# Kernel optimization log

Hardware: AMD Instinct MI355X
Metric: run time of the kernel (lower is better)

Reference implementation:

```python
import jax, jax.numpy as jnp
import numpy as np

DIM = 1024
HDS = 16
HEAD_DIM = DIM // HDS
ISC = True


def setup_inputs() -> dict:
    key = jax.random.key(0)
    k = jax.random.split(key, 5)
    x = jax.random.normal(k[0], (4, 2048, DIM), dtype=jnp.float32)
    # Linear(dim, 3*dim): weight [3*dim, dim] (torch layout), bias [3*dim]
    scale = 1.0 / np.sqrt(DIM)
    w_qkv = jax.random.uniform(k[1], (3 * DIM, DIM), jnp.float32, -scale, scale)
    b_qkv = jax.random.uniform(k[2], (3 * DIM,), jnp.float32, -scale, scale)
    w_out = jax.random.uniform(k[3], (DIM, DIM), jnp.float32, -scale, scale)
    b_out = jax.random.uniform(k[4], (DIM,), jnp.float32, -scale, scale)
    return {"x": x, "w_qkv": w_qkv, "b_qkv": b_qkv, "w_out": w_out, "b_out": b_out}


def reference(x, w_qkv, b_qkv, w_out, b_out):
    b, s, dim = x.shape
    # QKV projection: x @ w_qkv.T + b_qkv -> split into q, k, v
    qkv = jnp.einsum('bsd,ed->bse', x, w_qkv) + b_qkv
    q, k, v = jnp.split(qkv, 3, axis=-1)
    # [b, s, dim] -> [b, h, s, hd]
    def to_heads(t):
        return t.reshape(b, s, HDS, HEAD_DIM).transpose(0, 2, 1, 3)
    q, k, v = to_heads(q), to_heads(k), to_heads(v)
    att = jnp.einsum('bhqd,bhkd->bhqk', q, k) * (HEAD_DIM ** -0.5)
    if ISC:
        mask = jnp.triu(jnp.ones((s, s), dtype=bool), k=1)  # True above diagonal
        att = jnp.where(mask[None, None], -jnp.inf, att)
    att = jax.nn.softmax(att, axis=-1)
    # dropout is identity in eval mode
    out = jnp.einsum('bhqk,bhkd->bhqd', att, v)
    out = out.transpose(0, 2, 1, 3).reshape(b, s, dim)
    out = jnp.einsum('bsd,ed->bse', out, w_out) + b_out
    return out
```

## Files before the change

kernel.cpp:

```cpp
#include <hip/hip_runtime.h>
#include <stdint.h>

typedef __bf16 bf16x8 __attribute__((ext_vector_type(8)));
typedef short s16x8 __attribute__((ext_vector_type(8)));
typedef short s16x4 __attribute__((ext_vector_type(4)));
typedef float f32x4 __attribute__((ext_vector_type(4)));
typedef unsigned short u16;

#define K_DIM 1024

static __device__ __forceinline__ u16 f2bf(float f) {
    uint32_t x = __float_as_uint(f);
    x += 0x7fffu + ((x >> 16) & 1u);
    return (u16)(x >> 16);
}

static __device__ __forceinline__ f32x4 mfma16(s16x8 a, s16x8 b, f32x4 c) {
    return __builtin_amdgcn_mfma_f32_16x16x32_bf16(
        __builtin_bit_cast(bf16x8, a), __builtin_bit_cast(bf16x8, b), c, 0, 0, 0);
}

static __device__ __forceinline__ void gload16(const u16* g, u16* l) {
    __builtin_amdgcn_global_load_lds(
        (const __attribute__((address_space(1))) void*)g,
        (__attribute__((address_space(3))) void*)l,
        16, 0, 0);
}

static __device__ __forceinline__ uint32_t cvt_pk_bf16(float lo, float hi) {
    uint32_t r;
    asm("v_cvt_pk_bf16_f32 %0, %1, %2" : "=v"(r) : "v"(lo), "v"(hi));
    return r;
}

static __device__ __forceinline__ float fexp2(float x) {
#if __has_builtin(__builtin_amdgcn_exp2f)
    return __builtin_amdgcn_exp2f(x);
#else
    return __expf(x * 0.69314718056f);
#endif
}

__global__ void cvt_all(const float* __restrict__ x, const float* __restrict__ wq,
                        const float* __restrict__ wo,
                        u16* __restrict__ xb, u16* __restrict__ wqb,
                        u16* __restrict__ wob) {
    const int stride = gridDim.x * blockDim.x;
    const int tid = blockIdx.x * blockDim.x + threadIdx.x;
    for (int i = tid; i < 2097152; i += stride) {
        float4 f = ((const float4*)x)[i];
        ushort4 o;
        o.x = f2bf(f.x); o.y = f2bf(f.y); o.z = f2bf(f.z); o.w = f2bf(f.w);
        ((ushort4*)xb)[i] = o;
    }
    for (int i = tid; i < 786432; i += stride) {
        float4 f = ((const float4*)wq)[i];
        ushort4 o;
        o.x = f2bf(f.x); o.y = f2bf(f.y); o.z = f2bf(f.z); o.w = f2bf(f.w);
        ((ushort4*)wqb)[i] = o;
    }
    for (int i = tid; i < 262144; i += stride) {
        float4 f = ((const float4*)wo)[i];
        ushort4 o;
        o.x = f2bf(f.x); o.y = f2bf(f.y); o.z = f2bf(f.z); o.w = f2bf(f.w);
        ((ushort4*)wob)[i] = o;
    }
}

__global__ __launch_bounds__(256) void gemm_qkv(
    const u16* __restrict__ A, const u16* __restrict__ B,
    const float* __restrict__ bias,
    u16* __restrict__ qo, u16* __restrict__ ko, u16* __restrict__ vto)
{
    __shared__ u16 smem[32768];
    u16* ct = smem;
    const int tid = threadIdx.x;
    const int w = tid >> 6, l = tid & 63;
    const int lr = l & 15, lc = l >> 4;

    const int f = blockIdx.y * 64 + blockIdx.x;
    const int c = f & 7, j = f >> 3;
    const int m0 = (c * 8 + (j & 7)) * 128;
    const int n0 = (j >> 3) * 128;
    const int wm = (w >> 1) * 64, wn = (w & 1) * 64;

    const int srow = w * 8 + (l >> 3);
    const int scol = ((l & 7) ^ (l >> 3)) * 8;
    const u16* gA = A + (size_t)(m0 + srow) * K_DIM + scol;
    const u16* gB = B + (size_t)(n0 + srow) * K_DIM + scol;

    f32x4 acc[4][4] = {};

    auto stage = [&](int k0, int buf) {
        u16* base = smem + buf * 16384;
        #pragma unroll
        for (int g = 0; g < 4; ++g) {
            gload16(gA + (size_t)g * 32 * K_DIM + k0, base + (g * 32 + w * 8) * 64);
            gload16(gB + (size_t)g * 32 * K_DIM + k0, base + 8192 + (g * 32 + w * 8) * 64);
        }
    };

    stage(0, 0);
    int cur = 0;

    for (int k0 = 0; k0 < K_DIM; k0 += 64) {
        __syncthreads();
        if (k0 + 64 < K_DIM) stage(k0 + 64, cur ^ 1);
        const u16* As = smem + cur * 16384;
        const u16* Bs = As + 8192;
        #pragma unroll
        for (int kk = 0; kk < 2; ++kk) {
            s16x8 a[4], b[4];
            #pragma unroll
            for (int i = 0; i < 4; ++i) {
                const int row = wm + i * 16 + lr;
                a[i] = *(const s16x8*)&As[row * 64 + ((kk * 32 + lc * 8) ^ ((row & 7) * 8))];
            }
            #pragma unroll
            for (int jn = 0; jn < 4; ++jn) {
                const int row = wn + jn * 16 + lr;
                b[jn] = *(const s16x8*)&Bs[row * 64 + ((kk * 32 + lc * 8) ^ ((row & 7) * 8))];
            }
            #pragma unroll
            for (int i = 0; i < 4; ++i)
                #pragma unroll
                for (int jn = 0; jn < 4; ++jn)
                    acc[i][jn] = mfma16(a[i], b[jn], acc[i][jn]);
        }
        cur ^= 1;
    }

    const int sec = n0 >> 10;
    const int bb = m0 >> 11, s0 = m0 & 2047;

    if (sec < 2) {
        #pragma unroll
        for (int jn = 0; jn < 4; ++jn) {
            const int n = n0 + wn + jn * 16 + lr;
            const float bv = bias[n];
            const int h = (n & 1023) >> 6, d = n & 63;
            #pragma unroll
            for (int i = 0; i < 4; ++i) {
                #pragma unroll
                for (int r = 0; r < 4; ++r) {
                    const int m = m0 + wm + i * 16 + lc * 4 + r;
                    const int s = m & 2047;
                    float v = acc[i][jn][r] + bv;
                    if (sec == 0)
                        qo[((size_t)((bb * 16 + h) * 2048 + s)) * 64 + d] = f2bf(v * 0.18033688f);
                    else
                        ko[((size_t)((bb * 16 + h) * 2048 + s)) * 64 + d] = f2bf(v);
                }
            }
        }
    } else {
        __syncthreads();
        #pragma unroll
        for (int jj = 0; jj < 4; ++jj) {
            const int nl = (wn >> 6) * 16 + lr;
            const float bv = bias[n0 + wn + jj * 16 + lr];
            #pragma unroll
            for (int i = 0; i < 4; ++i) {
                const int mloc = wm + i * 16 + lc * 4;
                uint2 pk;
                pk.x = cvt_pk_bf16(acc[i][jj][0] + bv, acc[i][jj][1] + bv);
                pk.y = cvt_pk_bf16(acc[i][jj][2] + bv, acc[i][jj][3] + bv);
                *(s16x4*)&ct[nl * 136 + mloc] = __builtin_bit_cast(s16x4, pk);
            }
            __syncthreads();
            #pragma unroll
            for (int rep = 0; rep < 2; ++rep) {
                const int col = tid >> 3;
                const int seg = (tid & 7) + rep * 8;
                const int nn = n0 + (col >> 4) * 64 + jj * 16 + (col & 15);
                const int h = (nn & 1023) >> 6, d = nn & 63;
                const int mo = seg * 8;
                s16x8 v = *(const s16x8*)&ct[col * 136 + mo];
                *(s16x8*)&vto[((size_t)((bb * 16 + h) * 64 + d)) * 2048 + s0 + mo] = v;
            }
            __syncthreads();
        }
    }
}

__global__ __launch_bounds__(256, 3) void attn_fwd(
    const u16* __restrict__ q, const u16* __restrict__ k,
    const u16* __restrict__ vt, u16* __restrict__ ao)
{
    __shared__ u16 kt[2][8 * 512];
    __shared__ u16 vtl[2][8 * 512];
    __shared__ u16 plds[4 * 32 * 72];
    const int w = threadIdx.x >> 6, l = threadIdx.x & 63;
    const int lr = l & 15, lc = l >> 4;
    const int bh = blockIdx.x;
    const int C = 15 - blockIdx.y;
    const u16* qp = q + (size_t)bh * 2048 * 64;
    const u16* kp = k + (size_t)bh * 2048 * 64;
    const u16* vp = vt + (size_t)bh * 64 * 2048;
    u16* pl = &plds[w * 2304];
    const int bb = bh >> 4, h = bh & 15;

    const int q0 = C * 128 + w * 32;
    const int nb = 2 * C + 2;
    const int diag = 2 * C + (w >> 1);

    s16x8 aQ[2][2];
    #pragma unroll
    for (int i = 0; i < 2; ++i)
        #pragma unroll
        for (int kk = 0; kk < 2; ++kk)
            aQ[i][kk] = *(const s16x8*)&qp[(q0 + i * 16 + lr) * 64 + kk * 32 + lc * 8];

    f32x4 O[2][4] = {};
    f32x4 lsv[2] = {};

    auto stage = [&](int t, int buf) {
        const int c0 = t * 64;
        if (w < 2) {
            #pragma unroll
            for (int gi = 0; gi < 4; ++gi) {
                const int g = w * 4 + gi;
                const int jx = g >> 1, kk = g & 1;
                gload16(kp + (c0 + jx * 16 + lr) * 64 + kk * 32 + lc * 8,
                        &kt[buf][g * 512]);
            }
        } else {
            #pragma unroll
            for (int gi = 0; gi < 4; ++gi) {
                const int g = (w - 2) * 4 + gi;
                const int jd = g >> 1, kk = g & 1;
                gload16(vp + (jd * 16 + lr) * 2048 + c0 + kk * 32 + lc * 8,
                        &vtl[buf][g * 512]);
            }
        }
    };

    stage(0, 0);
    int cur = 0;

    for (int t = 0; t < nb; ++t) {
        __syncthreads();
        if (t + 1 < nb) stage(t + 1, cur ^ 1);

        if (t <= diag) {
            const int c0 = t * 64;
            f32x4 s[2][4] = {};
            __builtin_amdgcn_s_setprio(1);
            #pragma unroll
            for (int jx = 0; jx < 4; ++jx) {
                s16x8 k0 = *(const s16x8*)&kt[cur][(jx * 2 + 0) * 512 + l * 8];
                s16x8 k1 = *(const s16x8*)&kt[cur][(jx * 2 + 1) * 512 + l * 8];
                s[0][jx] = mfma16(k0, aQ[0][0], s[0][jx]);
                s[0][jx] = mfma16(k1, aQ[0][1], s[0][jx]);
                s[1][jx] = mfma16(k0, aQ[1][0], s[1][jx]);
                s[1][jx] = mfma16(k1, aQ[1][1], s[1][jx]);
            }
            __builtin_amdgcn_s_setprio(0);
            s16x8 vf[4][2];
            #pragma unroll
            for (int jd = 0; jd < 4; ++jd)
                #pragma unroll
                for (int kk = 0; kk < 2; ++kk)
                    vf[jd][kk] = *(const s16x8*)&vtl[cur][(jd * 2 + kk) * 512 + l * 8];
            if (t == diag) {
                #pragma unroll
                for (int i = 0; i < 2; ++i) {
                    const int qrow = q0 + i * 16 + lr;
                    #pragma unroll
                    for (int jx = 0; jx < 4; ++jx) {
                        const int kvb = c0 + jx * 16 + lc * 4;
                        #pragma unroll
                        for (int r = 0; r < 4; ++r)
                            if (kvb + r > qrow) s[i][jx][r] = -1e30f;
                    }
                }
            }
            #pragma unroll
            for (int i = 0; i < 2; ++i) {
                #pragma unroll
                for (int jx = 0; jx < 4; ++jx)
                    #pragma unroll
                    for (int r = 0; r < 4; ++r)
                        s[i][jx][r] = fexp2(s[i][jx][r]);
                lsv[i] += (s[i][0] + s[i][1]) + (s[i][2] + s[i][3]);
                #pragma unroll
                for (int jx = 0; jx < 4; ++jx) {
                    uint2 pk;
                    pk.x = cvt_pk_bf16(s[i][jx][0], s[i][jx][1]);
                    pk.y = cvt_pk_bf16(s[i][jx][2], s[i][jx][3]);
                    *(s16x4*)&pl[(i * 16 + lr) * 72 + jx * 16 + lc * 4] =
                        __builtin_bit_cast(s16x4, pk);
                }
            }
            s16x8 aP[2][2];
            #pragma unroll
            for (int i = 0; i < 2; ++i)
                #pragma unroll
                for (int kk = 0; kk < 2; ++kk)
                    aP[i][kk] = *(const s16x8*)&pl[(i * 16 + lr) * 72 + kk * 32 + lc * 8];
            __builtin_amdgcn_s_setprio(1);
            #pragma unroll
            for (int jd = 0; jd < 4; ++jd) {
                O[0][jd] = mfma16(aP[0][0], vf[jd][0], O[0][jd]);
                O[0][jd] = mfma16(aP[0][1], vf[jd][1], O[0][jd]);
                O[1][jd] = mfma16(aP[1][0], vf[jd][0], O[1][jd]);
                O[1][jd] = mfma16(aP[1][1], vf[jd][1], O[1][jd]);
            }
            __builtin_amdgcn_s_setprio(0);
        }
        cur ^= 1;
    }

    float lsr[2];
    #pragma unroll
    for (int i = 0; i < 2; ++i) {
        float t2 = (lsv[i][0] + lsv[i][1]) + (lsv[i][2] + lsv[i][3]);
        t2 += __shfl_xor(t2, 16);
        t2 += __shfl_xor(t2, 32);
        lsr[i] = 1.0f / t2;
    }
    float inv[2][4];
    #pragma unroll
    for (int i = 0; i < 2; ++i)
        #pragma unroll
        for (int r = 0; r < 4; ++r)
            inv[i][r] = __shfl(lsr[i], lc * 4 + r);

    #pragma unroll
    for (int i = 0; i < 2; ++i)
        #pragma unroll
        for (int jd = 0; jd < 4; ++jd)
            #pragma unroll
            for (int r = 0; r < 4; ++r) {
                const int srow = q0 + i * 16 + lc * 4 + r;
                ao[((size_t)(bb * 2048 + srow)) * 1024 + h * 64 + jd * 16 + lr] =
                    f2bf(O[i][jd][r] * inv[i][r]);
            }
}

__global__ __launch_bounds__(256) void gemm_out(
    const u16* __restrict__ A, const u16* __restrict__ B,
    const float* __restrict__ bias, float* __restrict__ out)
{
    __shared__ u16 smem[32768];
    const int tid = threadIdx.x;
    const int w = tid >> 6, l = tid & 63;
    const int lr = l & 15, lc = l >> 4;

    const int f = blockIdx.y * 64 + blockIdx.x;
    const int c = f & 7, j = f >> 3;
    const int m0 = (c * 8 + (j & 7)) * 128;
    const int n0 = (j >> 3) * 128;
    const int wm = (w >> 1) * 64, wn = (w & 1) * 64;

    const int srow = w * 8 + (l >> 3);
    const int scol = ((l & 7) ^ (l >> 3)) * 8;
    const u16* gA = A + (size_t)(m0 + srow) * K_DIM + scol;
    const u16* gB = B + (size_t)(n0 + srow) * K_DIM + scol;

    f32x4 acc[4][4] = {};

    auto stage = [&](int k0, int buf) {
        u16* base = smem + buf * 16384;
        #pragma unroll
        for (int g = 0; g < 4; ++g) {
            gload16(gA + (size_t)g * 32 * K_DIM + k0, base + (g * 32 + w * 8) * 64);
            gload16(gB + (size_t)g * 32 * K_DIM + k0, base + 8192 + (g * 32 + w * 8) * 64);
        }
    };

    stage(0, 0);
    int cur = 0;

    for (int k0 = 0; k0 < K_DIM; k0 += 64) {
        __syncthreads();
        if (k0 + 64 < K_DIM) stage(k0 + 64, cur ^ 1);
        const u16* As = smem + cur * 16384;
        const u16* Bs = As + 8192;
        #pragma unroll
        for (int kk = 0; kk < 2; ++kk) {
            s16x8 a[4], b[4];
            #pragma unroll
            for (int i = 0; i < 4; ++i) {
                const int row = wm + i * 16 + lr;
                a[i] = *(const s16x8*)&As[row * 64 + ((kk * 32 + lc * 8) ^ ((row & 7) * 8))];
            }
            #pragma unroll
            for (int jn = 0; jn < 4; ++jn) {
                const int row = wn + jn * 16 + lr;
                b[jn] = *(const s16x8*)&Bs[row * 64 + ((kk * 32 + lc * 8) ^ ((row & 7) * 8))];
            }
            #pragma unroll
            for (int i = 0; i < 4; ++i)
                #pragma unroll
                for (int jn = 0; jn < 4; ++jn)
                    acc[i][jn] = mfma16(a[i], b[jn], acc[i][jn]);
        }
        cur ^= 1;
    }

    #pragma unroll
    for (int jn = 0; jn < 4; ++jn) {
        const int n = n0 + wn + jn * 16 + lr;
        const float bv = bias[n];
        #pragma unroll
        for (int i = 0; i < 4; ++i) {
            #pragma unroll
            for (int r = 0; r < 4; ++r) {
                const int m = m0 + wm + i * 16 + lc * 4 + r;
                out[(size_t)m * 1024 + n] = acc[i][jn][r] + bv;
            }
        }
    }
}

extern "C" void kernel_launch(void* const* d_in, const int* in_sizes, int n_in,
                              void* d_out, int out_size, void* d_ws, size_t ws_size,
                              hipStream_t stream) {
    const float* x     = (const float*)d_in[0];
    const float* w_qkv = (const float*)d_in[1];
    const float* b_qkv = (const float*)d_in[2];
    const float* w_out = (const float*)d_in[3];
    const float* b_out = (const float*)d_in[4];
    float* out = (float*)d_out;

    char* ws = (char*)d_ws;
    u16* xb   = (u16*)(ws);
    u16* wqb  = (u16*)(ws + 16777216);
    u16* wob  = (u16*)(ws + 23068672);
    u16* qws  = (u16*)(ws + 25165824);
    u16* kws  = (u16*)(ws + 41943040);
    u16* vtws = (u16*)(ws + 58720256);
    u16* attn = (u16*)(ws + 75497472);

    cvt_all<<<dim3(2048), 256, 0, stream>>>(x, w_qkv, w_out, xb, wqb, wob);

    gemm_qkv<<<dim3(64, 24), 256, 0, stream>>>(xb, wqb, b_qkv, qws, kws, vtws);
    attn_fwd<<<dim3(64, 16), 256, 0, stream>>>(qws, kws, vtws, attn);
    gemm_out<<<dim3(64, 8), 256, 0, stream>>>(attn, wob, b_out, out);
}
```

Measured before the change: 135.1 us.

## Use two waves per attention block with 64 query rows each

After: 140.8 us. +4.2%, slower.

```diff
diff --git a/kernel.cpp b/kernel.cpp
--- a/kernel.cpp
+++ b/kernel.cpp
@@ -183,13 +183,13 @@
     }
 }
 
-__global__ __launch_bounds__(256, 3) void attn_fwd(
+__global__ __launch_bounds__(128, 2) void attn_fwd(
     const u16* __restrict__ q, const u16* __restrict__ k,
     const u16* __restrict__ vt, u16* __restrict__ ao)
 {
     __shared__ u16 kt[2][8 * 512];
     __shared__ u16 vtl[2][8 * 512];
-    __shared__ u16 plds[4 * 32 * 72];
+    __shared__ u16 plds[2 * 64 * 72];
     const int w = threadIdx.x >> 6, l = threadIdx.x & 63;
     const int lr = l & 15, lc = l >> 4;
     const int bh = blockIdx.x;
@@ -197,37 +197,35 @@
     const u16* qp = q + (size_t)bh * 2048 * 64;
     const u16* kp = k + (size_t)bh * 2048 * 64;
     const u16* vp = vt + (size_t)bh * 64 * 2048;
-    u16* pl = &plds[w * 2304];
+    u16* pl = &plds[w * 64 * 72];
     const int bb = bh >> 4, h = bh & 15;
 
-    const int q0 = C * 128 + w * 32;
+    const int q0 = C * 128 + w * 64;
     const int nb = 2 * C + 2;
-    const int diag = 2 * C + (w >> 1);
-
-    s16x8 aQ[2][2];
+    const int diag = 2 * C + w;
+
+    s16x8 aQ[4][2];
     #pragma unroll
-    for (int i = 0; i < 2; ++i)
+    for (int i = 0; i < 4; ++i)
         #pragma unroll
         for (int kk = 0; kk < 2; ++kk)
             aQ[i][kk] = *(const s16x8*)&qp[(q0 + i * 16 + lr) * 64 + kk * 32 + lc * 8];
 
-    f32x4 O[2][4] = {};
-    f32x4 lsv[2] = {};
+    f32x4 O[4][4] = {};
+    f32x4 lsv[4] = {};
 
     auto stage = [&](int t, int buf) {
         const int c0 = t * 64;
-        if (w < 2) {
-            #pragma unroll
-            for (int gi = 0; gi < 4; ++gi) {
-                const int g = w * 4 + gi;
+        if (w == 0) {
+            #pragma unroll
+            for (int g = 0; g < 8; ++g) {
                 const int jx = g >> 1, kk = g & 1;
                 gload16(kp + (c0 + jx * 16 + lr) * 64 + kk * 32 + lc * 8,
                         &kt[buf][g * 512]);
             }
         } else {
             #pragma unroll
-            for (int gi = 0; gi < 4; ++gi) {
-                const int g = (w - 2) * 4 + gi;
+            for (int g = 0; g < 8; ++g) {
                 const int jd = g >> 1, kk = g & 1;
                 gload16(vp + (jd * 16 + lr) * 2048 + c0 + kk * 32 + lc * 8,
                         &vtl[buf][g * 512]);
@@ -244,27 +242,22 @@
 
         if (t <= diag) {
             const int c0 = t * 64;
-            f32x4 s[2][4] = {};
+            f32x4 s[4][4] = {};
             __builtin_amdgcn_s_setprio(1);
             #pragma unroll
             for (int jx = 0; jx < 4; ++jx) {
                 s16x8 k0 = *(const s16x8*)&kt[cur][(jx * 2 + 0) * 512 + l * 8];
                 s16x8 k1 = *(const s16x8*)&kt[cur][(jx * 2 + 1) * 512 + l * 8];
-                s[0][jx] = mfma16(k0, aQ[0][0], s[0][jx]);
-                s[0][jx] = mfma16(k1, aQ[0][1], s[0][jx]);
-                s[1][jx] = mfma16(k0, aQ[1][0], s[1][jx]);
-                s[1][jx] = mfma16(k1, aQ[1][1], s[1][jx]);
+                #pragma unroll
+                for (int i = 0; i < 4; ++i) {
+                    s[i][jx] = mfma16(k0, aQ[i][0], s[i][jx]);
+                    s[i][jx] = mfma16(k1, aQ[i][1], s[i][jx]);
+                }
             }
             __builtin_amdgcn_s_setprio(0);
-            s16x8 vf[4][2];
-            #pragma unroll
-            for (int jd = 0; jd < 4; ++jd)
-                #pragma unroll
-                for (int kk = 0; kk < 2; ++kk)
-                    vf[jd][kk] = *(const s16x8*)&vtl[cur][(jd * 2 + kk) * 512 + l * 8];
             if (t == diag) {
                 #pragma unroll
-                for (int i = 0; i < 2; ++i) {
+                for (int i = 0; i < 4; ++i) {
                     const int qrow = q0 + i * 16 + lr;
                     #pragma unroll
                     for (int jx = 0; jx < 4; ++jx) {
@@ -276,7 +269,7 @@
                 }
             }
             #pragma unroll
-            for (int i = 0; i < 2; ++i) {
+            for (int i = 0; i < 4; ++i) {
                 #pragma unroll
                 for (int jx = 0; jx < 4; ++jx)
                     #pragma unroll
@@ -292,42 +285,41 @@
                         __builtin_bit_cast(s16x4, pk);
                 }
             }
-            s16x8 aP[2][2];
-            #pragma unroll
-            for (int i = 0; i < 2; ++i)
-                #pragma unroll
-                for (int kk = 0; kk < 2; ++kk)
-                    aP[i][kk] = *(const s16x8*)&pl[(i * 16 + lr) * 72 + kk * 32 + lc * 8];
             __builtin_amdgcn_s_setprio(1);
             #pragma unroll
             for (int jd = 0; jd < 4; ++jd) {
-                O[0][jd] = mfma16(aP[0][0], vf[jd][0], O[0][jd]);
-                O[0][jd] = mfma16(aP[0][1], vf[jd][1], O[0][jd]);
-                O[1][jd] = mfma16(aP[1][0], vf[jd][0], O[1][jd]);
-                O[1][jd] = mfma16(aP[1][1], vf[jd][1], O[1][jd]);
+                s16x8 v0 = *(const s16x8*)&vtl[cur][(jd * 2 + 0) * 512 + l * 8];
+                s16x8 v1 = *(const s16x8*)&vtl[cur][(jd * 2 + 1) * 512 + l * 8];
+                #pragma unroll
+                for (int i = 0; i < 4; ++i) {
+                    s16x8 aP0 = *(const s16x8*)&pl[(i * 16 + lr) * 72 + 0 * 32 + lc * 8];
+                    s16x8 aP1 = *(const s16x8*)&pl[(i * 16 + lr) * 72 + 1 * 32 + lc * 8];
+                    O[i][jd] = mfma16(aP0, v0, O[i][jd]);
+                    O[i][jd] = mfma16(aP1, v1, O[i][jd]);
+                }
             }
             __builtin_amdgcn_s_setprio(0);
         }
         cur ^= 1;
     }
 
-    float lsr[2];
+    float lsr[4];
     #pragma unroll
-    for (int i = 0; i < 2; ++i) {
+    for (int i = 0; i < 4; ++i) {
         float t2 = (lsv[i][0] + lsv[i][1]) + (lsv[i][2] + lsv[i][3]);
         t2 += __shfl_xor(t2, 16);
         t2 += __shfl_xor(t2, 32);
         lsr[i] = 1.0f / t2;
     }
-    float inv[2][4];
+    float inv[4][4];
     #pragma unroll
-    for (int i = 0; i < 2; ++i)
+    for (int i = 0; i < 4; ++i)
         #pragma unroll
         for (int r = 0; r < 4; ++r)
             inv[i][r] = __shfl(lsr[i], lc * 4 + r);
 
     #pragma unroll
-    for (int i = 0; i < 2; ++i)
+    for (int i = 0; i < 4; ++i)
         #pragma unroll
         for (int jd = 0; jd < 4; ++jd)
             #pragma unroll
@@ -436,6 +428,6 @@
     cvt_all<<<dim3(2048), 256, 0, stream>>>(x, w_qkv, w_out, xb, wqb, wob);
 
     gemm_qkv<<<dim3(64, 24), 256, 0, stream>>>(xb, wqb, b_qkv, qws, kws, vtws);
-    attn_fwd<<<dim3(64, 16), 256, 0, stream>>>(qws, kws, vtws, attn);
+    attn_fwd<<<dim3(64, 16), 128, 0, stream>>>(qws, kws, vtws, attn);
     gemm_out<<<dim3(64, 8), 256, 0, stream>>>(attn, wob, b_out, out);
 }
```
